# Optimization experiments

Measured on AMD Instinct MI355X. Metric: run time of the kernel, lower is better.

Reference implementation:

```python
import jax, jax.numpy as jnp
import numpy as np

B, N = 256, 400
DIMENSIONS, VOCAB = 400, 2
T_DIM, H_DIM = 128, 256
EDGE_P = 0.05
LOG_MAX_POS = np.float32(np.log(10000.0))


def timestep_embedding(t, dim):
    # transformer sinusoidal embedding (DDPM/score-SDE style)
    half = dim // 2
    freqs = jnp.exp(-LOG_MAX_POS * jnp.arange(half, dtype=jnp.float32) / (half - 1))
    args = t[:, None] * freqs[None, :]  # [B, half]
    return jnp.concatenate([jnp.sin(args), jnp.cos(args)], axis=-1)  # [B, dim]


def gcn_norm_adj(adj):
    # PyG GCNConv: binary edges (dense_to_sparse values discarded), add self loops,
    # symmetric normalization. deg computed per target (column sums).
    A = (adj != 0).astype(adj.dtype)
    eye = jnp.eye(adj.shape[-1], dtype=adj.dtype)
    As = A + eye[None]                     # [B,N,N]
    deg = As.sum(axis=-2)                  # column sums, [B,N]; >=1 due to self loops
    dis = 1.0 / jnp.sqrt(deg)              # [B,N]
    # out[i] = dis[i] * sum_j As[j,i] * dis[j] * x[j]  ->  An = dis_i * As^T * dis_j
    return dis[:, :, None] * jnp.swapaxes(As, -1, -2) * dis[:, None, :]


def setup_inputs() -> dict:
    key = jax.random.key(0)
    k = jax.random.split(key, 8)
    # symmetric Bernoulli adjacency, no self loops
    up = jnp.triu(jax.random.bernoulli(k[0], EDGE_P, (B, N, N)), 1)
    adj = (up + jnp.swapaxes(up, -1, -2)).astype(jnp.float32)
    times = jax.random.uniform(k[1], (B,), dtype=jnp.float32)
    s = 0.05
    W1 = jax.random.normal(k[2], (T_DIM + 1, H_DIM), jnp.float32) * s
    b1 = jnp.zeros((H_DIM,), jnp.float32)
    W2 = jax.random.normal(k[3], (H_DIM, H_DIM), jnp.float32) * s
    b2 = jnp.zeros((H_DIM,), jnp.float32)
    Wlin = jax.random.normal(k[4], (H_DIM, DIMENSIONS * VOCAB), jnp.float32) * s
    blin = jnp.zeros((DIMENSIONS * VOCAB,), jnp.float32)
    return {"adj": adj, "times": times, "W1": W1, "b1": b1,
            "W2": W2, "b2": b2, "Wlin": Wlin, "blin": blin}


def reference(adj, times, W1, b1, W2, b2, Wlin, blin):
    b, n, _ = adj.shape
    node_degree = adj.sum(axis=1)[..., None]                     # [B,N,1]
    temb = timestep_embedding(times, T_DIM)                      # [B,T_DIM]
    temb = jnp.broadcast_to(temb[:, None, :], (b, n, T_DIM))     # [B,N,T_DIM]
    x = jnp.concatenate([node_degree, temb], axis=-1)            # [B,N,T_DIM+1]

    An = gcn_norm_adj(adj)                                       # [B,N,N]
    h = jnp.einsum('bij,bjh->bih', An, x @ W1) + b1              # GCNConv 1
    h = jax.nn.relu(h)
    h = jnp.einsum('bij,bjh->bih', An, h @ W2) + b2              # GCNConv 2
    h = jax.nn.relu(h)
    pooled = h.mean(axis=1)                                      # global mean pool [B,H]
    logits = pooled @ Wlin + blin                                # [B, D*V]
    return logits.reshape(b, DIMENSIONS, VOCAB)
```

## Files before the change

### kernel.cpp

```cpp
#include <hip/hip_runtime.h>
#include <cstdint>
#include <cstddef>

#define BATCH 256
#define NN 400
#define HH 256
#define TDIM 128
#define HALFD 64
#define OUTD 800
#define BITW 16
#define BMW 13
#define W2PAD 264
#define Y2S 416

using short8  = __attribute__((ext_vector_type(8))) short;
using short4v = __attribute__((ext_vector_type(4))) short;
using f32x4   = __attribute__((ext_vector_type(4))) float;

__device__ __forceinline__ short f2bf_trunc(float x) {
  union { float f; unsigned int u; } c; c.f = x; return (short)(c.u >> 16);
}
__device__ __forceinline__ short f2bf_rne(float x) {
  union { float f; unsigned int u; } c; c.f = x;
  unsigned int r = c.u + 0x7FFFu + ((c.u >> 16) & 1u);
  return (short)(r >> 16);
}

__global__ __launch_bounds__(256) void k_prep(const float* __restrict__ adj,
    unsigned int* __restrict__ bits, float* __restrict__ dis,
    float* __restrict__ dd) {
  int bg = blockIdx.x;
  int rbase = blockIdx.y * 16;
  int wv = threadIdx.x >> 6, lane = threadIdx.x & 63;
#pragma unroll
  for (int rr = 0; rr < 4; ++rr) {
    int i = rbase + wv * 4 + rr;
    const float* arow = adj + ((size_t)bg * NN + i) * NN;
    unsigned int b8 = 0; int c = 0;
    if (lane < 50) {
      float4 v0 = *(const float4*)(arow + 8 * lane);
      float4 v1 = *(const float4*)(arow + 8 * lane + 4);
      b8 = (v0.x != 0.f ? 1u : 0u) | (v0.y != 0.f ? 2u : 0u) |
           (v0.z != 0.f ? 4u : 0u) | (v0.w != 0.f ? 8u : 0u) |
           (v1.x != 0.f ? 16u : 0u) | (v1.y != 0.f ? 32u : 0u) |
           (v1.z != 0.f ? 64u : 0u) | (v1.w != 0.f ? 128u : 0u);
      c = __popc(b8);
      if ((i >> 3) == lane) b8 |= 1u << (i & 7);
    }
    int cs = c;
#pragma unroll
    for (int s = 32; s; s >>= 1) cs += __shfl_xor(cs, s);
    unsigned int p0 = (unsigned int)__shfl((int)b8, 4 * lane);
    unsigned int p1 = (unsigned int)__shfl((int)b8, 4 * lane + 1);
    unsigned int p2 = (unsigned int)__shfl((int)b8, 4 * lane + 2);
    unsigned int p3 = (unsigned int)__shfl((int)b8, 4 * lane + 3);
    if (lane < BITW)
      bits[((size_t)bg * NN + i) * BITW + lane] =
          (lane < BMW) ? (p0 | (p1 << 8) | (p2 << 16) | (p3 << 24)) : 0u;
    if (lane == 0) {
      float d = rsqrtf((float)cs + 1.f);
      dis[bg * NN + i] = d;
      dd[bg * NN + i] = d * (float)cs;
    }
  }
}

__global__ __launch_bounds__(256) void k_temb(
    const float* __restrict__ times, const float* __restrict__ W1,
    float* __restrict__ tproj) {
  int b = blockIdx.x, t = threadIdx.x;
  __shared__ float te[TDIM];
  if (t < HALFD) {
    float f = expf(-9.210340371976184f * (float)t / (float)(HALFD - 1));
    float arg = times[b] * f;
    te[t] = sinf(arg);
    te[t + HALFD] = cosf(arg);
  }
  __syncthreads();
  float acc = 0.f;
#pragma unroll 8
  for (int k = 0; k < TDIM; ++k) acc += te[k] * W1[(1 + k) * HH + t];
  tproj[b * HH + t] = acc;
}

__global__ __launch_bounds__(256) void k_w2t(const float* __restrict__ W2,
                                             short* __restrict__ W2Tg) {
  int n = blockIdx.x, k = threadIdx.x;
  W2Tg[n * W2PAD + k] = f2bf_rne(W2[k * HH + n]);
}

__global__ __launch_bounds__(512) void k_pq(const unsigned int* __restrict__ bits,
    const float* __restrict__ dis, const float* __restrict__ dd,
    float* __restrict__ pp, float* __restrict__ qq) {
  int bg = blockIdx.x, t = threadIdx.x;
  __shared__ float sd[NN], su[NN];
  for (int j = t; j < NN; j += 512) { sd[j] = dis[bg * NN + j]; su[j] = dd[bg * NN + j]; }
  __syncthreads();
  if (t >= NN) return;
  const uint4* bp = (const uint4*)(bits + ((size_t)bg * NN + t) * BITW);
  uint4 qa = bp[0], qb = bp[1], qc = bp[2];
  unsigned int wr[13] = {qa.x, qa.y, qa.z, qa.w, qb.x, qb.y, qb.z, qb.w,
                         qc.x, qc.y, qc.z, qc.w, ((const unsigned int*)bp)[12]};
  float ps = 0.f, qs = 0.f;
#pragma unroll
  for (int w = 0; w < BMW; ++w) {
    unsigned int u = wr[w];
    int base = w * 32;
    while (u) {
      int j = base + __builtin_ctz(u);
      u &= u - 1;
      ps += su[j]; qs += sd[j];
    }
  }
  float d = sd[t];
  pp[bg * NN + t] = d * ps;
  qq[bg * NN + t] = d * qs;
}

__global__ __launch_bounds__(512, 2) void k_fused(
    const unsigned int* __restrict__ bits, const float* __restrict__ disg,
    const float* __restrict__ ppg, const float* __restrict__ qqg,
    const short* __restrict__ W2Tg, const float* __restrict__ W1,
    const float* __restrict__ b1, const float* __restrict__ tproj,
    const float* __restrict__ b2, float* __restrict__ pooled) {
  extern __shared__ char smem[];
  short* w2tq        = (short*)smem;
  short* y2q         = (short*)(smem + 33792);
  unsigned int* bmpL = (unsigned int*)(smem + 87040);
  float* sd          = (float*)(smem + 107840);
  float* ppL         = (float*)(smem + 109440);
  float* qqL         = (float*)(smem + 111040);
  float* pool        = (float*)(smem + 112640);

  int t = threadIdx.x;
  int wv = t >> 6, lane = t & 63, l15 = lane & 15, l4 = lane >> 4;
  int bg = blockIdx.x, q = blockIdx.y;

#pragma unroll
  for (int i = 0; i < 5; ++i) {
    int idx = i * 512 + t;
    if (idx < 2112) {
      int n = idx / 33, c = idx % 33;
      *(short8*)(w2tq + n * W2PAD + c * 8) =
          *(const short8*)(W2Tg + (size_t)(q * 64 + n) * W2PAD + c * 8);
    }
  }
  if (t < NN) {
    const uint4* bp = (const uint4*)(bits + ((size_t)bg * NN + t) * BITW);
    uint4 qa = bp[0], qb = bp[1], qc = bp[2];
    bmpL[t * BMW + 0] = qa.x;  bmpL[t * BMW + 1] = qa.y;
    bmpL[t * BMW + 2] = qa.z;  bmpL[t * BMW + 3] = qa.w;
    bmpL[t * BMW + 4] = qb.x;  bmpL[t * BMW + 5] = qb.y;
    bmpL[t * BMW + 6] = qb.z;  bmpL[t * BMW + 7] = qb.w;
    bmpL[t * BMW + 8] = qc.x;  bmpL[t * BMW + 9] = qc.y;
    bmpL[t * BMW + 10] = qc.z; bmpL[t * BMW + 11] = qc.w;
    bmpL[t * BMW + 12] = ((const unsigned int*)bp)[12];
    sd[t] = disg[bg * NN + t];
    ppL[t] = ppg[bg * NN + t];
    qqL[t] = qqg[bg * NN + t];
  }
  if (t < 128) {
    int n = t >> 1, c = t & 1;
    short8 z = {};
    *(short8*)(y2q + n * Y2S + 400 + c * 8) = z;
  }
  __syncthreads();

  const float* tpr = tproj + bg * HH;
  float pv[4], qv[4];
#pragma unroll
  for (int mi = 0; mi < 4; ++mi) {
    int mt = wv + mi * 8;
    int arow = mt * 16 + l15;
    pv[mi] = (mt < 25) ? ppL[arow] : 0.f;
    qv[mi] = (mt < 25) ? qqL[arow] : 0.f;
  }
  f32x4 acc[4][4];
#pragma unroll
  for (int mi = 0; mi < 4; ++mi)
#pragma unroll
    for (int f = 0; f < 4; ++f) acc[mi][f] = (f32x4){0.f, 0.f, 0.f, 0.f};

#pragma unroll
  for (int k0 = 0; k0 < 8; ++k0) {
    int kk = k0 * 32 + l4 * 8;
    float4 w1a = *(const float4*)(W1 + kk), w1b = *(const float4*)(W1 + kk + 4);
    float4 b1a = *(const float4*)(b1 + kk), b1b = *(const float4*)(b1 + kk + 4);
    float4 tpa = *(const float4*)(tpr + kk), tpb = *(const float4*)(tpr + kk + 4);
    short8 bf[4];
#pragma unroll
    for (int f = 0; f < 4; ++f)
      bf[f] = *(const short8*)(w2tq + (f * 16 + l15) * W2PAD + kk);
#pragma unroll
    for (int mi = 0; mi < 4; ++mi) {
      if (wv + mi * 8 < 25) {
        float ppv = pv[mi], qqv = qv[mi];
        short8 af;
        af[0] = f2bf_trunc(fmaxf(ppv * w1a.x + qqv * tpa.x + b1a.x, 0.f));
        af[1] = f2bf_trunc(fmaxf(ppv * w1a.y + qqv * tpa.y + b1a.y, 0.f));
        af[2] = f2bf_trunc(fmaxf(ppv * w1a.z + qqv * tpa.z + b1a.z, 0.f));
        af[3] = f2bf_trunc(fmaxf(ppv * w1a.w + qqv * tpa.w + b1a.w, 0.f));
        af[4] = f2bf_trunc(fmaxf(ppv * w1b.x + qqv * tpb.x + b1b.x, 0.f));
        af[5] = f2bf_trunc(fmaxf(ppv * w1b.y + qqv * tpb.y + b1b.y, 0.f));
        af[6] = f2bf_trunc(fmaxf(ppv * w1b.z + qqv * tpb.z + b1b.z, 0.f));
        af[7] = f2bf_trunc(fmaxf(ppv * w1b.w + qqv * tpb.w + b1b.w, 0.f));
#pragma unroll
        for (int f = 0; f < 4; ++f)
          acc[mi][f] = __builtin_amdgcn_mfma_f32_16x16x32_bf16(af, bf[f], acc[mi][f], 0, 0, 0);
      }
    }
  }
#pragma unroll
  for (int mi = 0; mi < 4; ++mi) {
    int mt = wv + mi * 8;
    if (mt < 25) {
      float4 d4 = *(const float4*)(sd + mt * 16 + l4 * 4);
#pragma unroll
      for (int f = 0; f < 4; ++f) {
        short4v pk;
        pk[0] = f2bf_trunc(d4.x * acc[mi][f][0]);
        pk[1] = f2bf_trunc(d4.y * acc[mi][f][1]);
        pk[2] = f2bf_trunc(d4.z * acc[mi][f][2]);
        pk[3] = f2bf_trunc(d4.w * acc[mi][f][3]);
        *(short4v*)(y2q + (f * 16 + l15) * Y2S + mt * 16 + l4 * 4) = pk;
      }
    }
  }
  __syncthreads();

  f32x4 acc2[4][4];
#pragma unroll
  for (int mi = 0; mi < 4; ++mi)
#pragma unroll
    for (int f = 0; f < 4; ++f) acc2[mi][f] = (f32x4){0.f, 0.f, 0.f, 0.f};

#pragma unroll
  for (int ks = 0; ks < 13; ++ks) {
    short8 bfv[4];
#pragma unroll
    for (int f = 0; f < 4; ++f)
      bfv[f] = *(const short8*)(y2q + (f * 16 + l15) * Y2S + ks * 32 + l4 * 8);
#pragma unroll
    for (int mi = 0; mi < 4; ++mi) {
      int mt = wv + mi * 8;
      if (mt < 25) {
        unsigned int wd = bmpL[(mt * 16 + l15) * BMW + ks];
        unsigned int byt = (wd >> (l4 * 8)) & 0xFFu;
        short8 af;
#pragma unroll
        for (int e = 0; e < 8; ++e)
          af[e] = (short)(((byt >> e) & 1u) * 0x3F80u);
#pragma unroll
        for (int f = 0; f < 4; ++f)
          acc2[mi][f] = __builtin_amdgcn_mfma_f32_16x16x32_bf16(af, bfv[f], acc2[mi][f], 0, 0, 0);
      }
    }
  }

#pragma unroll
  for (int f = 0; f < 4; ++f) {
    float b2v = b2[q * 64 + f * 16 + l15];
    float s = 0.f;
#pragma unroll
    for (int mi = 0; mi < 4; ++mi) {
      int mt = wv + mi * 8;
      if (mt < 25) {
        float4 d4 = *(const float4*)(sd + mt * 16 + l4 * 4);
        s += fmaxf(d4.x * acc2[mi][f][0] + b2v, 0.f)
           + fmaxf(d4.y * acc2[mi][f][1] + b2v, 0.f)
           + fmaxf(d4.z * acc2[mi][f][2] + b2v, 0.f)
           + fmaxf(d4.w * acc2[mi][f][3] + b2v, 0.f);
      }
    }
    s += __shfl_xor(s, 16);
    s += __shfl_xor(s, 32);
    if (l4 == 0) pool[wv * 64 + f * 16 + l15] = s;
  }
  __syncthreads();
  if (t < 64) {
    float sum = 0.f;
#pragma unroll
    for (int w8 = 0; w8 < 8; ++w8) sum += pool[w8 * 64 + t];
    pooled[(size_t)bg * HH + q * 64 + t] = sum;
  }
}

__global__ __launch_bounds__(256) void k_out(
    const float* __restrict__ pooled, const float* __restrict__ Wlin,
    const float* __restrict__ blin, float* __restrict__ out) {
  int bb = blockIdx.x * 2, t = threadIdx.x;
  __shared__ float ps[2][HH];
  ps[0][t] = pooled[(size_t)bb * HH + t] * (1.f / 400.f);
  ps[1][t] = pooled[(size_t)(bb + 1) * HH + t] * (1.f / 400.f);
  __syncthreads();
#pragma unroll
  for (int c = 0; c < 4; ++c) {
    int o = t + c * 256;
    if (o < OUTD) {
      float a0 = blin[o], a1 = a0;
#pragma unroll 8
      for (int h = 0; h < HH; ++h) {
        float wv = Wlin[h * OUTD + o];
        a0 += ps[0][h] * wv;
        a1 += ps[1][h] * wv;
      }
      out[(size_t)bb * OUTD + o] = a0;
      out[(size_t)(bb + 1) * OUTD + o] = a1;
    }
  }
}

extern "C" void kernel_launch(void* const* d_in, const int* in_sizes, int n_in,
                              void* d_out, int out_size, void* d_ws, size_t ws_size,
                              hipStream_t stream) {
  const float* adj   = (const float*)d_in[0];
  const float* times = (const float*)d_in[1];
  const float* W1    = (const float*)d_in[2];
  const float* b1    = (const float*)d_in[3];
  const float* W2    = (const float*)d_in[4];
  const float* b2    = (const float*)d_in[5];
  const float* Wlin  = (const float*)d_in[6];
  const float* blin  = (const float*)d_in[7];
  float* out = (float*)d_out;

  char* ws = (char*)d_ws;
  size_t off = 0;
  auto alloc = [&](size_t bytes) -> void* {
    void* ptr = ws + off;
    off = (off + bytes + 255) & ~(size_t)255;
    return ptr;
  };
  float* dis    = (float*)alloc((size_t)BATCH * NN * 4);
  float* dd     = (float*)alloc((size_t)BATCH * NN * 4);
  float* pp     = (float*)alloc((size_t)BATCH * NN * 4);
  float* qq     = (float*)alloc((size_t)BATCH * NN * 4);
  float* tproj  = (float*)alloc((size_t)BATCH * HH * 4);
  float* pooled = (float*)alloc((size_t)BATCH * HH * 4);
  short* W2Tg   = (short*)alloc((size_t)HH * W2PAD * 2);
  unsigned int* bits = (unsigned int*)alloc((size_t)BATCH * NN * BITW * 4);

  k_temb<<<BATCH, 256, 0, stream>>>(times, W1, tproj);
  k_w2t<<<HH, 256, 0, stream>>>(W2, W2Tg);
  k_prep<<<dim3(BATCH, 25), 256, 0, stream>>>(adj, bits, dis, dd);
  k_pq<<<BATCH, 512, 0, stream>>>(bits, dis, dd, pp, qq);
  k_fused<<<dim3(BATCH, 4), 512, 114688, stream>>>(
      bits, dis, pp, qq, W2Tg, W1, b1, tproj, b2, pooled);
  k_out<<<128, 256, 0, stream>>>(pooled, Wlin, blin, out);
}
```

Baseline: 161.3 us.

## Pre-swizzle W2 into MFMA fragment order and read B operands from global

The W2 transpose kernel now writes bf16 W2 directly in per-lane MFMA B-fragment order, so each wave reads its B fragments with one coalesced short8 load from global/L2. The fused kernel no longer stages a 64x264 W2 slice in LDS, which removes the copy loop and cuts shared memory from about 112KB to about 79KB per block. This may allow more blocks per CU, but it moves B-operand reads from LDS onto the L2 cache path inside the K loop.

```diff
diff --git a/kernel.cpp b/kernel.cpp
--- a/kernel.cpp
+++ b/kernel.cpp
@@ -10,7 +10,6 @@
 #define OUTD 800
 #define BITW 16
 #define BMW 13
-#define W2PAD 264
 #define Y2S 416
 
 using short8  = __attribute__((ext_vector_type(8))) short;
@@ -83,10 +82,18 @@
   tproj[b * HH + t] = acc;
 }
 
-__global__ __launch_bounds__(256) void k_w2t(const float* __restrict__ W2,
-                                             short* __restrict__ W2Tg) {
-  int n = blockIdx.x, k = threadIdx.x;
-  W2Tg[n * W2PAD + k] = f2bf_rne(W2[k * HH + n]);
+__global__ __launch_bounds__(256) void k_w2s(const float* __restrict__ W2,
+                                             short* __restrict__ W2s) {
+  int t = threadIdx.x;
+  int blk = blockIdx.x * 4 + (t >> 6);
+  int lane = t & 63;
+  int q = blk >> 5, k0 = (blk >> 2) & 7, f = blk & 3;
+  int n = q * 64 + f * 16 + (lane & 15);
+  int kb = k0 * 32 + (lane >> 4) * 8;
+  short8 v;
+#pragma unroll
+  for (int e = 0; e < 8; ++e) v[e] = f2bf_rne(W2[(size_t)(kb + e) * HH + n]);
+  *(short8*)(W2s + (size_t)blk * 512 + lane * 8) = v;
 }
 
 __global__ __launch_bounds__(512) void k_pq(const unsigned int* __restrict__ bits,
@@ -120,31 +127,21 @@
 __global__ __launch_bounds__(512, 2) void k_fused(
     const unsigned int* __restrict__ bits, const float* __restrict__ disg,
     const float* __restrict__ ppg, const float* __restrict__ qqg,
-    const short* __restrict__ W2Tg, const float* __restrict__ W1,
+    const short* __restrict__ W2s, const float* __restrict__ W1,
     const float* __restrict__ b1, const float* __restrict__ tproj,
     const float* __restrict__ b2, float* __restrict__ pooled) {
   extern __shared__ char smem[];
-  short* w2tq        = (short*)smem;
-  short* y2q         = (short*)(smem + 33792);
-  unsigned int* bmpL = (unsigned int*)(smem + 87040);
-  float* sd          = (float*)(smem + 107840);
-  float* ppL         = (float*)(smem + 109440);
-  float* qqL         = (float*)(smem + 111040);
-  float* pool        = (float*)(smem + 112640);
+  short* y2q         = (short*)smem;
+  unsigned int* bmpL = (unsigned int*)(smem + 53248);
+  float* sd          = (float*)(smem + 74048);
+  float* ppL         = (float*)(smem + 75648);
+  float* qqL         = (float*)(smem + 77248);
+  float* pool        = (float*)(smem + 78848);
 
   int t = threadIdx.x;
   int wv = t >> 6, lane = t & 63, l15 = lane & 15, l4 = lane >> 4;
   int bg = blockIdx.x, q = blockIdx.y;
 
-#pragma unroll
-  for (int i = 0; i < 5; ++i) {
-    int idx = i * 512 + t;
-    if (idx < 2112) {
-      int n = idx / 33, c = idx % 33;
-      *(short8*)(w2tq + n * W2PAD + c * 8) =
-          *(const short8*)(W2Tg + (size_t)(q * 64 + n) * W2PAD + c * 8);
-    }
-  }
   if (t < NN) {
     const uint4* bp = (const uint4*)(bits + ((size_t)bg * NN + t) * BITW);
     uint4 qa = bp[0], qb = bp[1], qc = bp[2];
@@ -167,6 +164,7 @@
   __syncthreads();
 
   const float* tpr = tproj + bg * HH;
+  const short* w2b = W2s + (size_t)q * 8 * 4 * 512;
   float pv[4], qv[4];
 #pragma unroll
   for (int mi = 0; mi < 4; ++mi) {
@@ -190,7 +188,7 @@
     short8 bf[4];
 #pragma unroll
     for (int f = 0; f < 4; ++f)
-      bf[f] = *(const short8*)(w2tq + (f * 16 + l15) * W2PAD + kk);
+      bf[f] = *(const short8*)(w2b + (size_t)(k0 * 4 + f) * 512 + lane * 8);
 #pragma unroll
     for (int mi = 0; mi < 4; ++mi) {
       if (wv + mi * 8 < 25) {
@@ -336,14 +334,14 @@
   float* qq     = (float*)alloc((size_t)BATCH * NN * 4);
   float* tproj  = (float*)alloc((size_t)BATCH * HH * 4);
   float* pooled = (float*)alloc((size_t)BATCH * HH * 4);
-  short* W2Tg   = (short*)alloc((size_t)HH * W2PAD * 2);
+  short* W2s    = (short*)alloc((size_t)128 * 512 * 2);
   unsigned int* bits = (unsigned int*)alloc((size_t)BATCH * NN * BITW * 4);
 
   k_temb<<<BATCH, 256, 0, stream>>>(times, W1, tproj);
-  k_w2t<<<HH, 256, 0, stream>>>(W2, W2Tg);
+  k_w2s<<<32, 256, 0, stream>>>(W2, W2s);
   k_prep<<<dim3(BATCH, 25), 256, 0, stream>>>(adj, bits, dis, dd);
   k_pq<<<BATCH, 512, 0, stream>>>(bits, dis, dd, pp, qq);
-  k_fused<<<dim3(BATCH, 4), 512, 114688, stream>>>(
-      bits, dis, pp, qq, W2Tg, W1, b1, tproj, b2, pooled);
+  k_fused<<<dim3(BATCH, 4), 512, 80896, stream>>>(
+      bits, dis, pp, qq, W2s, W1, b1, tproj, b2, pooled);
   k_out<<<128, 256, 0, stream>>>(pooled, Wlin, blin, out);
 }
```

After: 158.6 us. No clear change (-1.7%).
